# Kernel optimization log

Measured on AMD Instinct MI355X. Metric: run time of the kernel, lower is better.

Reference implementation:

```python
import jax, jax.numpy as jnp
import numpy as np

N = 131072          # num MCMC chains (num_samples)
N_STEPS = 60        # sample_mcmc default n_steps
EPS_INIT = 10.0     # sample_mcmc default eps_init
H = 128             # hidden width of the energy MLP


def setup_inputs() -> dict:
    key = jax.random.key(0)
    ks = jax.random.split(key, 8)
    d = {}
    # init points uniform in [-1, 1] (mimics the fresh-sample branch / buffer contents)
    d["x0"] = jax.random.uniform(ks[0], (N, 2), jnp.float32, minval=-1.0, maxval=1.0)
    # MLP 2 -> 128 -> 128 -> 128 -> 128 -> 1 (Kaiming-ish scale)
    def init_w(k, shape):
        fan_in = shape[0]
        return jax.random.normal(k, shape, jnp.float32) / jnp.sqrt(jnp.float32(fan_in))
    d["w1"] = init_w(ks[1], (2, H));  d["b1"] = jnp.zeros((H,), jnp.float32)
    d["w2"] = init_w(ks[2], (H, H));  d["b2"] = jnp.zeros((H,), jnp.float32)
    d["w3"] = init_w(ks[3], (H, H));  d["b3"] = jnp.zeros((H,), jnp.float32)
    d["w4"] = init_w(ks[4], (H, H));  d["b4"] = jnp.zeros((H,), jnp.float32)
    d["w5"] = init_w(ks[5], (H, 1));  d["b5"] = jnp.zeros((1,), jnp.float32)
    # pre-drawn Langevin noise for each of the 60 steps (torch.randn_like per step)
    d["noise"] = jax.random.normal(ks[6], (N_STEPS, N, 2), jnp.float32)
    return d


def _energy(x, params):
    # nn.Sequential(Linear, SiLU, Linear, SiLU, Linear, SiLU, Linear, SiLU, Linear)
    w1, b1, w2, b2, w3, b3, w4, b4, w5, b5 = params
    h = jax.nn.silu(x @ w1 + b1)
    h = jax.nn.silu(h @ w2 + b2)
    h = jax.nn.silu(h @ w3 + b3)
    h = jax.nn.silu(h @ w4 + b4)
    return h @ w5 + b5  # [N, 1]


def reference(x0, w1, b1, w2, b2, w3, b3, w4, b4, w5, b5, noise):
    params = (w1, b1, w2, b2, w3, b3, w4, b4, w5, b5)
    # grad of sum of energies wrt x == per-sample dE/dx
    grad_fn = jax.grad(lambda x: _energy(x, params).sum())

    def step(x, inp):
        i, nz = inp
        eps = EPS_INIT * (1.0 - i / N_STEPS)  # eps_init - eps_init*step/n_steps
        # torch.autograd.grad (create_graph=False) -> detached grad
        g = jnp.clip(jax.lax.stop_gradient(grad_fn(x)), -0.03, 0.03)
        x = jnp.clip(x + jnp.sqrt(2.0 * eps) * nz * 0.005 + eps * g, -2.43, 3.05)
        return x, None

    steps = jnp.arange(N_STEPS, dtype=jnp.float32)
    x, _ = jax.lax.scan(step, x0, (steps, noise))
    return x
```

## Files before the change

kernel.cpp:

```cpp
#include <hip/hip_runtime.h>
#include <stdint.h>

#define NTOT    131072
#define NSTEP   60
#define SBLK    64
#define NBLK    (NTOT / SBLK)
#define PLANE_H 16384
#define IMG_H   32768
#define BPLANE_H 8192

#define OFF_ACT  0
#define OFF_GP   32768
#define OFF_W1C  34816
#define OFF_B2   36864
#define OFF_B3   37376
#define OFF_B4   37888
#define OFF_W5   38400
#define OFF_XB   38912
#define LDS_TOTAL 39424

typedef float  f32x4  __attribute__((ext_vector_type(4)));
typedef float  f32x16 __attribute__((ext_vector_type(16)));
typedef short  bf16x8 __attribute__((ext_vector_type(8)));
union FragU { bf16x8 v; uint32_t u[4]; uint16_t h[8]; };

static __device__ __forceinline__ uint32_t rne_bits(float f) {
  uint32_t u = __float_as_uint(f);
  return u + 0x7fffu + ((u >> 16) & 1u);
}
static __device__ __forceinline__ float fsigm(float z) {
  return __builtin_amdgcn_rcpf(1.0f + __builtin_amdgcn_exp2f(z * -1.44269504089f));
}
static __device__ __forceinline__ uint32_t cvt_pk_bf16(float a, float b) {
  uint32_t r;
  asm("v_cvt_pk_bf16_f32 %0, %1, %2" : "=v"(r) : "v"(a), "v"(b));
  return r;
}

extern "C" __global__ void ebm_prep_kernel(const float* __restrict__ w2,
                                           const float* __restrict__ w3,
                                           const float* __restrict__ w4,
                                           uint16_t* __restrict__ ws) {
  int img = blockIdx.x;
  bool bwd = img >= 3;
  int li = bwd ? 5 - img : img;
  const float* w = (li == 0) ? w2 : (li == 1) ? w3 : w4;
  uint16_t* hiP = ws + (size_t)img * IMG_H;
  uint16_t* loP = hiP + PLANE_H;
  for (int e = threadIdx.x; e < 16384; e += blockDim.x) {
    int i = e >> 7, o = e & 127;
    int m = bwd ? i : o;
    int k = bwd ? o : i;
    int slot = ((m >> 5) * 8 + (k >> 4)) * 64 + (m & 31) + 32 * ((k >> 3) & 1);
    int off = slot * 8 + (k & 7);
    float v = w[e];
    uint32_t tb = rne_bits(v);
    float lo = v - __uint_as_float(tb & 0xffff0000u);
    hiP[off] = (uint16_t)(tb >> 16);
    loP[off] = (uint16_t)(rne_bits(lo) >> 16);
  }
}

extern "C" __global__ void __launch_bounds__(512, 2)
ebm_mcmc_kernel(const float* __restrict__ x0, const float* __restrict__ w1,
                const float* __restrict__ b1, const float* __restrict__ b2,
                const float* __restrict__ b3, const float* __restrict__ b4,
                const float* __restrict__ w5, const float* __restrict__ noise,
                const uint16_t* __restrict__ wsW, float* __restrict__ out)
{
  extern __shared__ char smem[];
  uint16_t* ACTH  = (uint16_t*)(smem + OFF_ACT);
  float*    GPf   = (float*)(smem + OFF_GP);
  f32x4*    W1C   = (f32x4*)(smem + OFF_W1C);
  float*    B2s   = (float*)(smem + OFF_B2);
  float*    B3s   = (float*)(smem + OFF_B3);
  float*    B4s   = (float*)(smem + OFF_B4);
  float*    W5s   = (float*)(smem + OFF_W5);
  float*    XB    = (float*)(smem + OFF_XB);

  const int t   = threadIdx.x;
  const int blk = blockIdx.x;

  if (t < 128) {
    f32x4 v; v.x = w1[t]; v.y = w1[128 + t]; v.z = b1[t]; v.w = 0.0f;
    W1C[t] = v;
    B2s[t] = b2[t]; B3s[t] = b3[t]; B4s[t] = b4[t]; W5s[t] = w5[t];
    XB[t] = x0[(size_t)blk * 128 + t];
  }

  const int lane = t & 63;
  const int wave = t >> 6;
  const int c32 = lane & 31;
  const int h   = lane >> 5;
  const int wr  = wave & 3;
  const int wsh = wave >> 2;

  size_t nbase = (size_t)blk * 128 + (t & 127);
  float nz = (t < 128) ? noise[nbase] : 0.0f;

  __syncthreads();

  f32x16 acc;
  float D1[16], D2[16], D3[16];

  auto gemm = [&](int img) {
    const uint16_t* ab = wsW + (size_t)img * IMG_H + (size_t)(wr * 4096 + lane * 8);
    acc = (f32x16)0.0f;
#pragma unroll
    for (int ks = 0; ks < 8; ++ks) {
      FragU Ah, Al;
      Ah.v = *(const bf16x8*)(ab + ks * 512);
      Al.v = *(const bf16x8*)(ab + ks * 512 + PLANE_H);
      const uint16_t* bp = ACTH + ((wsh * 8 + ks) * 64 + lane) * 8;
      FragU Bh, Bl;
      Bh.v = *(const bf16x8*)bp;
      Bl.v = *(const bf16x8*)(bp + BPLANE_H);
      acc = __builtin_amdgcn_mfma_f32_32x32x16_bf16(Ah.v, Bh.v, acc, 0, 0, 0);
      acc = __builtin_amdgcn_mfma_f32_32x32x16_bf16(Ah.v, Bl.v, acc, 0, 0, 0);
      acc = __builtin_amdgcn_mfma_f32_32x32x16_bf16(Al.v, Bh.v, acc, 0, 0, 0);
    }
  };

  auto storeAct = [&](int tt, f32x4 v) {
    uint32_t h01 = cvt_pk_bf16(v[0], v[1]);
    uint32_t h23 = cvt_pk_bf16(v[2], v[3]);
    float r0 = v[0] - __uint_as_float(h01 << 16);
    float r1 = v[1] - __uint_as_float(h01 & 0xffff0000u);
    float r2 = v[2] - __uint_as_float(h23 << 16);
    float r3 = v[3] - __uint_as_float(h23 & 0xffff0000u);
    int slot = (wsh * 8 + 2 * wr + (tt >> 1)) * 64 + c32 + 32 * (tt & 1);
    uint16_t* p = ACTH + slot * 8 + 4 * h;
    *(uint2*)p = make_uint2(h01, h23);
    *(uint2*)(p + BPLANE_H) = make_uint2(cvt_pk_bf16(r0, r1), cvt_pk_bf16(r2, r3));
  };

  auto ep_fwd = [&](const float* Bs, float* D) {
#pragma unroll
    for (int tt = 0; tt < 4; ++tt) {
      f32x4 bv = *(const f32x4*)(Bs + 32 * wr + 8 * tt + 4 * h);
      f32x4 hv;
#pragma unroll
      for (int rr = 0; rr < 4; ++rr) {
        float z = acc[4 * tt + rr] + bv[rr];
        float s = fsigm(z);
        float hh = z * s;
        D[4 * tt + rr] = s * (1.0f + z - hh);
        hv[rr] = hh;
      }
      storeAct(tt, hv);
    }
  };

  auto ep_v4 = [&]() {
#pragma unroll
    for (int tt = 0; tt < 4; ++tt) {
      f32x4 bv = *(const f32x4*)(B4s + 32 * wr + 8 * tt + 4 * h);
      f32x4 wv = *(const f32x4*)(W5s + 32 * wr + 8 * tt + 4 * h);
      f32x4 vv;
#pragma unroll
      for (int rr = 0; rr < 4; ++rr) {
        float z = acc[4 * tt + rr] + bv[rr];
        float s = fsigm(z);
        vv[rr] = wv[rr] * (s * (1.0f + z - z * s));
      }
      storeAct(tt, vv);
    }
  };

  auto ep_bwd = [&](float* D) {
#pragma unroll
    for (int tt = 0; tt < 4; ++tt) {
      f32x4 vv;
#pragma unroll
      for (int rr = 0; rr < 4; ++rr)
        vv[rr] = acc[4 * tt + rr] * D[4 * tt + rr];
      storeAct(tt, vv);
    }
  };

  auto ep_bwd1 = [&]() {
    float gx = 0.f, gy = 0.f;
#pragma unroll
    for (int tt = 0; tt < 4; ++tt) {
      const f32x4* wp = W1C + 32 * wr + 8 * tt + 4 * h;
#pragma unroll
      for (int rr = 0; rr < 4; ++rr) {
        f32x4 w = wp[rr];
        float v = acc[4 * tt + rr] * D1[4 * tt + rr];
        gx = fmaf(v, w.x, gx);
        gy = fmaf(v, w.y, gy);
      }
    }
    gx += __shfl_xor(gx, 32);
    gy += __shfl_xor(gy, 32);
    if (h == 0) {
      int s = 32 * wsh + c32;
      *(float2*)(GPf + (wr * 64 + s) * 2) = make_float2(gx, gy);
    }
  };

  auto l1_phase = [&]() {
    float2 xv = *(const float2*)(XB + 2 * (32 * wsh + c32));
#pragma unroll
    for (int tt = 0; tt < 4; ++tt) {
      const f32x4* wp = W1C + 32 * wr + 8 * tt + 4 * h;
      f32x4 hv;
#pragma unroll
      for (int rr = 0; rr < 4; ++rr) {
        f32x4 w = wp[rr];
        float z = fmaf(xv.x, w.x, fmaf(xv.y, w.y, w.z));
        float s = fsigm(z);
        float hh = z * s;
        D1[4 * tt + rr] = s * (1.0f + z - hh);
        hv[rr] = hh;
      }
      storeAct(tt, hv);
    }
  };

  auto g_finish = [&](int step) {
    if (t < 128) {
      float g = GPf[t] + GPf[128 + t] + GPf[256 + t] + GPf[384 + t];
      g = fminf(fmaxf(g, -0.03f), 0.03f);
      float epsv = 10.0f * (1.0f - (float)step / 60.0f);
      float xn = XB[t] + sqrtf(2.0f * epsv) * nz * 0.005f + epsv * g;
      xn = fminf(fmaxf(xn, -2.43f), 3.05f);
      XB[t] = xn;
      if (step == NSTEP - 1) {
        out[(size_t)blk * 128 + t] = xn;
      } else {
        nz = noise[(size_t)(step + 1) * NTOT * 2 + nbase];
      }
    }
  };

#pragma unroll 1
  for (int step = 0; step < NSTEP; ++step) {
    l1_phase();        __syncthreads();
    gemm(0);           __syncthreads();
    ep_fwd(B2s, D2);   __syncthreads();
    gemm(1);           __syncthreads();
    ep_fwd(B3s, D3);   __syncthreads();
    gemm(2);           __syncthreads();
    ep_v4();           __syncthreads();
    gemm(3);           __syncthreads();
    ep_bwd(D3);        __syncthreads();
    gemm(4);           __syncthreads();
    ep_bwd(D2);        __syncthreads();
    gemm(5);           __syncthreads();
    ep_bwd1();         __syncthreads();
    g_finish(step);    __syncthreads();
  }
}

extern "C" void kernel_launch(void* const* d_in, const int* in_sizes, int n_in,
                              void* d_out, int out_size, void* d_ws, size_t ws_size,
                              hipStream_t stream) {
  (void)in_sizes; (void)n_in; (void)out_size; (void)ws_size;
  hipFuncSetAttribute((const void*)ebm_mcmc_kernel,
                      hipFuncAttributeMaxDynamicSharedMemorySize, LDS_TOTAL);
  ebm_prep_kernel<<<6, 256, 0, stream>>>(
      (const float*)d_in[3], (const float*)d_in[5], (const float*)d_in[7],
      (uint16_t*)d_ws);
  ebm_mcmc_kernel<<<NBLK, 512, LDS_TOTAL, stream>>>(
      (const float*)d_in[0], (const float*)d_in[1], (const float*)d_in[2],
      (const float*)d_in[4], (const float*)d_in[6], (const float*)d_in[8],
      (const float*)d_in[9], (const float*)d_in[11], (const uint16_t*)d_ws,
      (float*)d_out);
}
```

Measured before the change: 5.882 ms.

## Halve block to 32 chains and ping-pong activation buffers to drop barriers

Each block now handles 32 chains with 256 threads instead of 64 chains with 512. It alternates between two LDS activation buffers, so each GEMM and the following epilogue run back-to-back without a barrier between them, which roughly halves the __syncthreads per step. Launch bounds move to 256 threads with 3 blocks per CU so more, smaller blocks can be resident. In exchange, every block reloads the same weight fragments from global or L2 for half as many chains, so weight traffic per chain doubles.

```diff
diff --git a/kernel.cpp b/kernel.cpp
--- a/kernel.cpp
+++ b/kernel.cpp
@@ -3,21 +3,23 @@
 
 #define NTOT    131072
 #define NSTEP   60
-#define SBLK    64
+#define SBLK    32
 #define NBLK    (NTOT / SBLK)
 #define PLANE_H 16384
 #define IMG_H   32768
-#define BPLANE_H 8192
-
-#define OFF_ACT  0
+#define BPLANE_H 4096
+#define ACT_H   8192
+
+#define OFF_ACT0 0
+#define OFF_ACT1 16384
 #define OFF_GP   32768
-#define OFF_W1C  34816
-#define OFF_B2   36864
-#define OFF_B3   37376
-#define OFF_B4   37888
-#define OFF_W5   38400
-#define OFF_XB   38912
-#define LDS_TOTAL 39424
+#define OFF_W1C  33792
+#define OFF_B2   35840
+#define OFF_B3   36352
+#define OFF_B4   36864
+#define OFF_W5   37376
+#define OFF_XB   37888
+#define LDS_TOTAL 38144
 
 typedef float  f32x4  __attribute__((ext_vector_type(4)));
 typedef float  f32x16 __attribute__((ext_vector_type(16)));
@@ -61,7 +63,7 @@
   }
 }
 
-extern "C" __global__ void __launch_bounds__(512, 2)
+extern "C" __global__ void __launch_bounds__(256, 3)
 ebm_mcmc_kernel(const float* __restrict__ x0, const float* __restrict__ w1,
                 const float* __restrict__ b1, const float* __restrict__ b2,
                 const float* __restrict__ b3, const float* __restrict__ b4,
@@ -69,7 +71,8 @@
                 const uint16_t* __restrict__ wsW, float* __restrict__ out)
 {
   extern __shared__ char smem[];
-  uint16_t* ACTH  = (uint16_t*)(smem + OFF_ACT);
+  uint16_t* ACT0  = (uint16_t*)(smem + OFF_ACT0);
+  uint16_t* ACT1  = (uint16_t*)(smem + OFF_ACT1);
   float*    GPf   = (float*)(smem + OFF_GP);
   f32x4*    W1C   = (f32x4*)(smem + OFF_W1C);
   float*    B2s   = (float*)(smem + OFF_B2);
@@ -85,25 +88,24 @@
     f32x4 v; v.x = w1[t]; v.y = w1[128 + t]; v.z = b1[t]; v.w = 0.0f;
     W1C[t] = v;
     B2s[t] = b2[t]; B3s[t] = b3[t]; B4s[t] = b4[t]; W5s[t] = w5[t];
-    XB[t] = x0[(size_t)blk * 128 + t];
   }
+  if (t < 64) XB[t] = x0[(size_t)blk * 64 + t];
 
   const int lane = t & 63;
   const int wave = t >> 6;
   const int c32 = lane & 31;
   const int h   = lane >> 5;
-  const int wr  = wave & 3;
-  const int wsh = wave >> 2;
-
-  size_t nbase = (size_t)blk * 128 + (t & 127);
-  float nz = (t < 128) ? noise[nbase] : 0.0f;
+  const int wr  = wave;
+
+  size_t nbase = (size_t)blk * 64 + (t & 63);
+  float nz = (t < 64) ? noise[nbase] : 0.0f;
 
   __syncthreads();
 
   f32x16 acc;
   float D1[16], D2[16], D3[16];
 
-  auto gemm = [&](int img) {
+  auto gemm = [&](int img, const uint16_t* AB) {
     const uint16_t* ab = wsW + (size_t)img * IMG_H + (size_t)(wr * 4096 + lane * 8);
     acc = (f32x16)0.0f;
 #pragma unroll
@@ -111,7 +113,7 @@
       FragU Ah, Al;
       Ah.v = *(const bf16x8*)(ab + ks * 512);
       Al.v = *(const bf16x8*)(ab + ks * 512 + PLANE_H);
-      const uint16_t* bp = ACTH + ((wsh * 8 + ks) * 64 + lane) * 8;
+      const uint16_t* bp = AB + (ks * 64 + lane) * 8;
       FragU Bh, Bl;
       Bh.v = *(const bf16x8*)bp;
       Bl.v = *(const bf16x8*)(bp + BPLANE_H);
@@ -121,20 +123,20 @@
     }
   };
 
-  auto storeAct = [&](int tt, f32x4 v) {
+  auto storeAct = [&](uint16_t* AB, int tt, f32x4 v) {
     uint32_t h01 = cvt_pk_bf16(v[0], v[1]);
     uint32_t h23 = cvt_pk_bf16(v[2], v[3]);
     float r0 = v[0] - __uint_as_float(h01 << 16);
     float r1 = v[1] - __uint_as_float(h01 & 0xffff0000u);
     float r2 = v[2] - __uint_as_float(h23 << 16);
     float r3 = v[3] - __uint_as_float(h23 & 0xffff0000u);
-    int slot = (wsh * 8 + 2 * wr + (tt >> 1)) * 64 + c32 + 32 * (tt & 1);
-    uint16_t* p = ACTH + slot * 8 + 4 * h;
+    int slot = (2 * wr + (tt >> 1)) * 64 + c32 + 32 * (tt & 1);
+    uint16_t* p = AB + slot * 8 + 4 * h;
     *(uint2*)p = make_uint2(h01, h23);
     *(uint2*)(p + BPLANE_H) = make_uint2(cvt_pk_bf16(r0, r1), cvt_pk_bf16(r2, r3));
   };
 
-  auto ep_fwd = [&](const float* Bs, float* D) {
+  auto ep_fwd = [&](const float* Bs, float* D, uint16_t* AB) {
 #pragma unroll
     for (int tt = 0; tt < 4; ++tt) {
       f32x4 bv = *(const f32x4*)(Bs + 32 * wr + 8 * tt + 4 * h);
@@ -147,11 +149,11 @@
         D[4 * tt + rr] = s * (1.0f + z - hh);
         hv[rr] = hh;
       }
-      storeAct(tt, hv);
-    }
-  };
-
-  auto ep_v4 = [&]() {
+      storeAct(AB, tt, hv);
+    }
+  };
+
+  auto ep_v4 = [&](uint16_t* AB) {
 #pragma unroll
     for (int tt = 0; tt < 4; ++tt) {
       f32x4 bv = *(const f32x4*)(B4s + 32 * wr + 8 * tt + 4 * h);
@@ -163,18 +165,18 @@
         float s = fsigm(z);
         vv[rr] = wv[rr] * (s * (1.0f + z - z * s));
       }
-      storeAct(tt, vv);
-    }
-  };
-
-  auto ep_bwd = [&](float* D) {
+      storeAct(AB, tt, vv);
+    }
+  };
+
+  auto ep_bwd = [&](float* D, uint16_t* AB) {
 #pragma unroll
     for (int tt = 0; tt < 4; ++tt) {
       f32x4 vv;
 #pragma unroll
       for (int rr = 0; rr < 4; ++rr)
         vv[rr] = acc[4 * tt + rr] * D[4 * tt + rr];
-      storeAct(tt, vv);
+      storeAct(AB, tt, vv);
     }
   };
 
@@ -194,13 +196,12 @@
     gx += __shfl_xor(gx, 32);
     gy += __shfl_xor(gy, 32);
     if (h == 0) {
-      int s = 32 * wsh + c32;
-      *(float2*)(GPf + (wr * 64 + s) * 2) = make_float2(gx, gy);
-    }
-  };
-
-  auto l1_phase = [&]() {
-    float2 xv = *(const float2*)(XB + 2 * (32 * wsh + c32));
+      *(float2*)(GPf + (wr * 32 + c32) * 2) = make_float2(gx, gy);
+    }
+  };
+
+  auto l1_phase = [&](uint16_t* AB) {
+    float2 xv = *(const float2*)(XB + 2 * c32);
 #pragma unroll
     for (int tt = 0; tt < 4; ++tt) {
       const f32x4* wp = W1C + 32 * wr + 8 * tt + 4 * h;
@@ -214,20 +215,20 @@
         D1[4 * tt + rr] = s * (1.0f + z - hh);
         hv[rr] = hh;
       }
-      storeAct(tt, hv);
+      storeAct(AB, tt, hv);
     }
   };
 
   auto g_finish = [&](int step) {
-    if (t < 128) {
-      float g = GPf[t] + GPf[128 + t] + GPf[256 + t] + GPf[384 + t];
+    if (t < 64) {
+      float g = GPf[t] + GPf[64 + t] + GPf[128 + t] + GPf[192 + t];
       g = fminf(fmaxf(g, -0.03f), 0.03f);
       float epsv = 10.0f * (1.0f - (float)step / 60.0f);
       float xn = XB[t] + sqrtf(2.0f * epsv) * nz * 0.005f + epsv * g;
       xn = fminf(fmaxf(xn, -2.43f), 3.05f);
       XB[t] = xn;
       if (step == NSTEP - 1) {
-        out[(size_t)blk * 128 + t] = xn;
+        out[(size_t)blk * 64 + t] = xn;
       } else {
         nz = noise[(size_t)(step + 1) * NTOT * 2 + nbase];
       }
@@ -236,20 +237,14 @@
 
 #pragma unroll 1
   for (int step = 0; step < NSTEP; ++step) {
-    l1_phase();        __syncthreads();
-    gemm(0);           __syncthreads();
-    ep_fwd(B2s, D2);   __syncthreads();
-    gemm(1);           __syncthreads();
-    ep_fwd(B3s, D3);   __syncthreads();
-    gemm(2);           __syncthreads();
-    ep_v4();           __syncthreads();
-    gemm(3);           __syncthreads();
-    ep_bwd(D3);        __syncthreads();
-    gemm(4);           __syncthreads();
-    ep_bwd(D2);        __syncthreads();
-    gemm(5);           __syncthreads();
-    ep_bwd1();         __syncthreads();
-    g_finish(step);    __syncthreads();
+    l1_phase(ACT0);                 __syncthreads();
+    gemm(0, ACT0); ep_fwd(B2s, D2, ACT1); __syncthreads();
+    gemm(1, ACT1); ep_fwd(B3s, D3, ACT0); __syncthreads();
+    gemm(2, ACT0); ep_v4(ACT1);           __syncthreads();
+    gemm(3, ACT1); ep_bwd(D3, ACT0);      __syncthreads();
+    gemm(4, ACT0); ep_bwd(D2, ACT1);      __syncthreads();
+    gemm(5, ACT1); ep_bwd1();             __syncthreads();
+    g_finish(step);                 __syncthreads();
   }
 }
 
@@ -262,7 +257,7 @@
   ebm_prep_kernel<<<6, 256, 0, stream>>>(
       (const float*)d_in[3], (const float*)d_in[5], (const float*)d_in[7],
       (uint16_t*)d_ws);
-  ebm_mcmc_kernel<<<NBLK, 512, LDS_TOTAL, stream>>>(
+  ebm_mcmc_kernel<<<NBLK, 256, LDS_TOTAL, stream>>>(
       (const float*)d_in[0], (const float*)d_in[1], (const float*)d_in[2],
       (const float*)d_in[4], (const float*)d_in[6], (const float*)d_in[8],
       (const float*)d_in[9], (const float*)d_in[11], (const uint16_t*)d_ws,
```

New measurement: 9.654 ms. 64.1% more time.
